# Optimization experiments

Measured on AMD Instinct MI355X. Metric: run time of the kernel, lower is better.

## Reference

```python
import jax, jax.numpy as jnp
import numpy as np

N = 100000   # num nodes
E = 1600000  # num edges
D = 128      # input_dim
K = 5        # APPNP propagation steps
EPS = 1e-8   # torch cosine_similarity eps


def setup_inputs() -> dict:
    key = jax.random.key(0)
    k1, k2, k3, k4 = jax.random.split(key, 4)
    x = jax.random.normal(k1, (N, D), jnp.float32)
    mask = jax.random.normal(k2, (N, 1), jnp.float32)
    edge_index = jax.random.randint(k3, (2, E), 0, N, dtype=jnp.int32)
    # init_t: orthogonal weight with gain sqrt(2), zero bias
    W = jax.nn.initializers.orthogonal(scale=2 ** 0.5)(k4, (D, D), jnp.float32)
    b = jnp.zeros((D,), jnp.float32)
    alpha = jnp.array(0.5, jnp.float32)
    return {"x": x, "mask": mask, "edge_index": edge_index, "W": W, "b": b, "alpha": alpha}


def reference(x, mask, edge_index, W, b, alpha):
    n = x.shape[0]
    # x_fn: Linear + Tanh
    h = jnp.tanh(x @ W.T + b)
    src, dst = edge_index[0], edge_index[1]
    hs, hd = h[src], h[dst]  # [E, D] gathers
    # torch F.cosine_similarity with eps-clamped norms
    dot = jnp.sum(hs * hd, axis=-1)
    ns = jnp.maximum(jnp.sqrt(jnp.sum(hs * hs, axis=-1)), EPS)
    nd = jnp.maximum(jnp.sqrt(jnp.sum(hd * hd, axis=-1)), EPS)
    edge_weights = jax.nn.relu(dot / (ns * nd))  # [E]

    fill = jax.nn.relu(mask)  # [N, 1]

    # PyG APPNP: gcn_norm with self loops (fill value 1.0)
    loops = jnp.arange(n, dtype=src.dtype)
    row = jnp.concatenate([src, loops])
    col = jnp.concatenate([dst, loops])
    w = jnp.concatenate([edge_weights, jnp.ones((n,), edge_weights.dtype)])
    deg = jax.ops.segment_sum(w, col, num_segments=n)
    dinv = jnp.where(deg > 0, jax.lax.rsqrt(jnp.maximum(deg, EPS)), 0.0)
    norm = dinv[row] * w * dinv[col]  # [E+N]

    # K-step APPNP: z <- (1-alpha) * A_hat z + alpha * fill
    z = fill
    for _ in range(K):
        agg = jax.ops.segment_sum(norm[:, None] * z[row], col, num_segments=n)
        z = (1.0 - alpha) * agg + alpha * fill
    return z, edge_weights
```

## Files before the change

kernel.cpp:

```cpp
#include <hip/hip_runtime.h>
#include <hip/hip_bf16.h>

typedef __attribute__((ext_vector_type(2))) float f32x2;
typedef __attribute__((ext_vector_type(4))) float f32x4;
typedef __attribute__((ext_vector_type(8))) short short8;

#define D 128
#define EPS 1e-8f
#define BSH 8
#define BSZ 256
#define SMAX 8000
#define OSH 12
#define OBK 4096

__device__ __forceinline__ unsigned int pkbf(float lo, float hi) {
    unsigned int r;
    asm("v_cvt_pk_bf16_f32 %0, %1, %2" : "=v"(r) : "v"(lo), "v"(hi));
    return r;
}

__device__ __forceinline__ float ftanh(float y) {
    float e = __builtin_amdgcn_exp2f(y * 2.885390082f);
    float r = __builtin_amdgcn_rcpf(e + 1.0f);
    return __builtin_fmaf(-2.0f, r, 1.0f);
}

__device__ __forceinline__ int dot4(unsigned int a, unsigned int b, int c) {
#if __has_builtin(__builtin_amdgcn_sdot4)
    return __builtin_amdgcn_sdot4((int)a, (int)b, c, false);
#else
    int r = c;
    r += (int)(char)(a) * (int)(char)(b);
    r += (int)(char)(a >> 8) * (int)(char)(b >> 8);
    r += (int)(char)(a >> 16) * (int)(char)(b >> 16);
    r += (int)(char)(a >> 24) * (int)(char)(b >> 24);
    return r;
#endif
}

__global__ __launch_bounds__(256) void k1_gemm_aux(const float* __restrict__ x,
                                                   const float* __restrict__ W,
                                                   const float* __restrict__ b,
                                                   signed char* __restrict__ hn8,
                                                   int N,
                                                   const float* __restrict__ mask,
                                                   float* __restrict__ fill,
                                                   const int* __restrict__ dst,
                                                   int* __restrict__ M,
                                                   int E, int nbk, int nblk, int chunk,
                                                   int gemmNB) {
    __shared__ char Wlds[D * D * 2];
    int tid = threadIdx.x;

    if (blockIdx.x >= gemmNB) {
        int baux = blockIdx.x - gemmNB;
        int* cnt = (int*)Wlds;
        for (int k = tid; k < nbk; k += 256) cnt[k] = 0;
        int fi = baux * 256 + tid;
        if (fi < N) fill[fi] = fmaxf(mask[fi], 0.0f);
        __syncthreads();
        int beg = baux * chunk, end = min(E, beg + chunk);
        for (int e = beg + tid; e < end; e += 256)
            atomicAdd(&cnt[dst[e] >> BSH], 1);
        __syncthreads();
        for (int k = tid; k < nbk; k += 256)
            M[k * nblk + baux] = cnt[k];
        return;
    }

#pragma unroll
    for (int c = 0; c < 8; ++c) {
        int i = c * 256 + tid;
        float4 lo = *(const float4*)(W + i * 8);
        float4 hi = *(const float4*)(W + i * 8 + 4);
        uint4 v;
        v.x = pkbf(lo.x, lo.y); v.y = pkbf(lo.z, lo.w);
        v.z = pkbf(hi.x, hi.y); v.w = pkbf(hi.z, hi.w);
        int byte = i << 4;
        int swz  = byte ^ (((byte >> 8) & 15) << 4);
        *(uint4*)(Wlds + swz) = v;
    }
    __syncthreads();

    int wave = tid >> 6;
    int lane = tid & 63;
    int l16  = lane & 15;
    int g    = lane >> 4;

    float bj[8];
#pragma unroll
    for (int j = 0; j < 8; ++j) bj[j] = b[j * 16 + l16];

    for (int tt = 0; tt < 2; ++tt) {
        int r0 = blockIdx.x * 128 + wave * 32 + tt * 16;
        int arow = r0 + l16;
        if (arow >= N) arow = N - 1;
        union { uint4 u; short8 s; } afr[4];
        const float* xp = x + (size_t)arow * D + g * 8;
#pragma unroll
        for (int kc = 0; kc < 4; ++kc) {
            float4 lo = *(const float4*)(xp + kc * 32);
            float4 hi = *(const float4*)(xp + kc * 32 + 4);
            afr[kc].u.x = pkbf(lo.x, lo.y);
            afr[kc].u.y = pkbf(lo.z, lo.w);
            afr[kc].u.z = pkbf(hi.x, hi.y);
            afr[kc].u.w = pkbf(hi.z, hi.w);
        }

        f32x4 acc[8];
#pragma unroll
        for (int j = 0; j < 8; ++j) acc[j] = (f32x4){0.f, 0.f, 0.f, 0.f};
#pragma unroll
        for (int j = 0; j < 8; ++j) {
#pragma unroll
            for (int kc = 0; kc < 4; ++kc) {
                int addr = (j * 16 + l16) * 256 + kc * 64 + g * 16;
                const short8* bp = (const short8*)(Wlds + (addr ^ (l16 << 4)));
                acc[j] = __builtin_amdgcn_mfma_f32_16x16x32_bf16(afr[kc].s, *bp, acc[j], 0, 0, 0);
            }
        }

        float sq[4] = {0.f, 0.f, 0.f, 0.f};
#pragma unroll
        for (int j = 0; j < 8; ++j) {
#pragma unroll
            for (int r = 0; r < 4; ++r) {
                float tv = ftanh(acc[j][r] + bj[j]);
                acc[j][r] = tv;
                sq[r] = __builtin_fmaf(tv, tv, sq[r]);
            }
        }
#pragma unroll
        for (int m = 1; m <= 8; m <<= 1) {
#pragma unroll
            for (int r = 0; r < 4; ++r) sq[r] += __shfl_xor(sq[r], m);
        }
#pragma unroll
        for (int r = 0; r < 4; ++r) {
            float inv = rsqrtf(fmaxf(sq[r], 1e-16f)) * 127.0f;
            int row = r0 + g * 4 + r;
            if (row < N) {
#pragma unroll
                for (int j = 0; j < 8; ++j) {
                    hn8[(size_t)row * D + j * 16 + l16] =
                        (signed char)__float2int_rn(acc[j][r] * inv);
                }
            }
        }
    }
}

__global__ __launch_bounds__(1024) void scan_blk(const int* __restrict__ cnt,
                                                 int* __restrict__ rp,
                                                 int* __restrict__ bsum, int nq) {
    __shared__ int wsum[16];
    __shared__ int sexcl[16];
    int tid = threadIdx.x, lane = tid & 63, wv = tid >> 6;
    int idx = blockIdx.x * 1024 + tid;
    int4 c = (idx < nq) ? ((const int4*)cnt)[idx] : make_int4(0, 0, 0, 0);
    int tsum = c.x + c.y + c.z + c.w;
    int incl = tsum;
#pragma unroll
    for (int m = 1; m < 64; m <<= 1) {
        int t = __shfl_up(incl, m);
        if (lane >= m) incl += t;
    }
    if (lane == 63) wsum[wv] = incl;
    __syncthreads();
    if (tid == 0) {
        int acc = 0;
#pragma unroll
        for (int k = 0; k < 16; ++k) { int t = wsum[k]; sexcl[k] = acc; acc += t; }
        bsum[blockIdx.x] = acc;
    }
    __syncthreads();
    int excl = sexcl[wv] + incl - tsum;
    if (idx < nq) {
        int4 r;
        r.x = excl; r.y = excl + c.x; r.z = r.y + c.y; r.w = r.z + c.z;
        ((int4*)rp)[idx] = r;
    }
}

__global__ __launch_bounds__(256) void scan_top(int* __restrict__ bsum,
                                                int* __restrict__ boff, int nbs,
                                                int* __restrict__ gcur, int nbk2) {
    for (int k = threadIdx.x; k < nbk2; k += 256) gcur[k] = k << OSH;
    if (threadIdx.x == 0) {
        int acc = 0;
        for (int k = 0; k < nbs; ++k) { int t = bsum[k]; boff[k] = acc; acc += t; }
    }
}

__global__ __launch_bounds__(256) void bscat_kernel(const int* __restrict__ src,
                                                    const int* __restrict__ dst,
                                                    const int* __restrict__ Mo,
                                                    const int* __restrict__ boff,
                                                    int2* __restrict__ ebuf,
                                                    int E, int nbk, int nblk, int chunk) {
    extern __shared__ int cur[];
    int b = blockIdx.x;
    for (int k = threadIdx.x; k < nbk; k += 256) {
        int e = k * nblk + b;
        cur[k] = Mo[e] + boff[e >> 12];
    }
    __syncthreads();
    int beg = b * chunk, end = min(E, beg + chunk);
    for (int e = beg + threadIdx.x; e < end; e += 256) {
        int d = dst[e];
        int k = d >> BSH;
        int p = atomicAdd(&cur[k], 1);
        ebuf[p] = make_int2(src[e], (e << BSH) | (d & (BSZ - 1)));
    }
}

__global__ __launch_bounds__(256) void binsort_kernel(const int* __restrict__ Mo,
                                                      const int* __restrict__ boff,
                                                      const int2* __restrict__ ebuf,
                                                      int* __restrict__ esrc,
                                                      int* __restrict__ eorig,
                                                      int* __restrict__ rp,
                                                      int E, int N, int nbk, int nblk) {
    extern __shared__ char smem[];
    int2* stage = (int2*)smem;
    int*  cnt   = (int*)(smem + SMAX * 8);
    int k = blockIdx.x;
    int eb = k * nblk;
    int base = Mo[eb] + boff[eb >> 12];
    int endb = E;
    if (k + 1 < nbk) {
        int e2 = (k + 1) * nblk;
        endb = Mo[e2] + boff[e2 >> 12];
    }
    int m = endb - base;
    if (m > SMAX) m = SMAX;

    if (threadIdx.x < BSZ) cnt[threadIdx.x] = 0;
    __syncthreads();
    for (int i = threadIdx.x; i < m; i += 256) {
        int2 v = ebuf[base + i];
        stage[i] = v;
        atomicAdd(&cnt[v.y & (BSZ - 1)], 1);
    }
    __syncthreads();
    if (threadIdx.x == 0) {
        int acc = 0;
#pragma unroll 8
        for (int t = 0; t < BSZ; ++t) { int c = cnt[t]; cnt[t] = acc; acc += c; }
    }
    __syncthreads();
    {
        int node = (k << BSH) + threadIdx.x;
        if (threadIdx.x < BSZ && node < N) rp[node] = base + cnt[threadIdx.x];
        if (k == nbk - 1 && threadIdx.x == 0) rp[N] = E;
    }
    __syncthreads();
    for (int i = threadIdx.x; i < m; i += 256) {
        int2 v = stage[i];
        int p = atomicAdd(&cnt[v.y & (BSZ - 1)], 1);
        esrc[base + p]  = v.x;
        eorig[base + p] = v.y >> BSH;
    }
}

__global__ __launch_bounds__(256) void weight_kernel(const int* __restrict__ rp,
                                                     const int* __restrict__ esrc,
                                                     const signed char* __restrict__ hn8,
                                                     float* __restrict__ warr,
                                                     float* __restrict__ dinv, int N) {
    const float SC = 1.0f / 16129.0f;
    int gid = (blockIdx.x * 256 + threadIdx.x) >> 3;
    int l   = threadIdx.x & 7;
    if (gid >= N) return;
    const uint4* hp = (const uint4*)hn8;
    uint4 dv = hp[(size_t)gid * 8 + l];
    int beg = rp[gid], end = rp[gid + 1];
    float sum = 0.f;
    int s = beg;
    for (; s + 7 < end; s += 8) {
        uint4 u[8];
        int dd[8];
#pragma unroll
        for (int q = 0; q < 8; ++q) u[q] = hp[(size_t)esrc[s + q] * 8 + l];
#pragma unroll
        for (int q = 0; q < 8; ++q) {
            int d0 = dot4(u[q].x, dv.x, 0); d0 = dot4(u[q].y, dv.y, d0);
            d0 = dot4(u[q].z, dv.z, d0);    d0 = dot4(u[q].w, dv.w, d0);
            dd[q] = d0;
        }
#pragma unroll
        for (int m = 4; m >= 1; m >>= 1) {
#pragma unroll
            for (int q = 0; q < 8; ++q) dd[q] += __shfl_xor(dd[q], m);
        }
        float wv[8];
#pragma unroll
        for (int q = 0; q < 8; ++q) {
            wv[q] = fmaxf((float)dd[q] * SC, 0.f);
            sum += wv[q];
        }
        if (l == 0) {
#pragma unroll
            for (int q = 0; q < 8; ++q) warr[s + q] = wv[q];
        }
    }
    for (; s < end; ++s) {
        uint4 u0 = hp[(size_t)esrc[s] * 8 + l];
        int d0 = dot4(u0.x, dv.x, 0); d0 = dot4(u0.y, dv.y, d0);
        d0 = dot4(u0.z, dv.z, d0);    d0 = dot4(u0.w, dv.w, d0);
#pragma unroll
        for (int m = 4; m >= 1; m >>= 1) d0 += __shfl_xor(d0, m);
        float w0 = fmaxf((float)d0 * SC, 0.f);
        if (l == 0) warr[s] = w0;
        sum += w0;
    }
    if (l == 0) dinv[gid] = rsqrtf(1.0f + sum);
}

__global__ __launch_bounds__(256) void k6_dscat_appnp1(const int* __restrict__ eorig,
                                                       const float* __restrict__ warr,
                                                       int* __restrict__ gcur,
                                                       int2* __restrict__ pbuf,
                                                       int E, int nbk2, int chunk,
                                                       int dscatNB,
                                                       const int* __restrict__ rp,
                                                       const int* __restrict__ esrc,
                                                       int2* __restrict__ pw,
                                                       const float* __restrict__ dinv,
                                                       const float* __restrict__ fill,
                                                       const float* __restrict__ alpha,
                                                       float* __restrict__ zout, int N) {
    if (blockIdx.x < dscatNB) {
        extern __shared__ char smem[];
        int2* stage = (int2*)smem;
        int*  hist  = (int*)(smem + (size_t)chunk * 8);
        int*  lcur  = hist + nbk2;
        int b = blockIdx.x;
        for (int k = threadIdx.x; k < nbk2; k += 256) hist[k] = 0;
        __syncthreads();
        int beg = b * chunk, end = min(E, beg + chunk), m = end - beg;
        for (int i = threadIdx.x; i < m; i += 256) {
            int o = eorig[beg + i];
            float w = warr[beg + i];
            stage[i] = make_int2(o, __float_as_int(w));
            atomicAdd(&hist[o >> OSH], 1);
        }
        __syncthreads();
        for (int k = threadIdx.x; k < nbk2; k += 256) {
            int c = hist[k];
            lcur[k] = c ? atomicAdd(&gcur[k], c) : 0;
        }
        __syncthreads();
        for (int i = threadIdx.x; i < m; i += 256) {
            int2 v = stage[i];
            int p = atomicAdd(&lcur[v.x >> OSH], 1);
            pbuf[p] = v;
        }
        return;
    }
    int t = (blockIdx.x - dscatNB) * 256 + threadIdx.x;
    int i = t >> 2, l = t & 3;
    if (i >= N) return;
    int beg = rp[i], end = rp[i + 1];
    float al = alpha[0];
    float oma = 1.0f - al;
    float di = dinv[i];
    float s = 0.f;
    for (int j = beg + l; j < end; j += 4) {
        int sr = esrc[j];
        float wf = oma * warr[j] * di * dinv[sr];
        pw[j] = make_int2(sr, __float_as_int(wf));
        s += wf * fill[sr];
    }
    s += __shfl_xor(s, 1);
    s += __shfl_xor(s, 2);
    if (l == 0) {
        float fi = fill[i];
        zout[i] = al * fi + oma * di * di * fi + s;
    }
}

__global__ __launch_bounds__(256) void k7_appnp2_dfin(const int* __restrict__ rp,
                                                      const int2* __restrict__ pw,
                                                      const float* __restrict__ dinv,
                                                      const float* __restrict__ fill,
                                                      const float* __restrict__ zin,
                                                      const float* __restrict__ alpha,
                                                      float* __restrict__ zout, int N,
                                                      int appnpNB,
                                                      const int2* __restrict__ pbuf,
                                                      float* __restrict__ ew, int E) {
    if (blockIdx.x >= appnpNB) {
        int bk = blockIdx.x - appnpNB;
        int base = bk << OSH;
        int m = min(OBK, E - base);
        for (int t = threadIdx.x; t < m; t += 256) {
            int2 v = pbuf[base + t];
            ew[v.x] = __int_as_float(v.y);
        }
        return;
    }
    int t = blockIdx.x * 256 + threadIdx.x;
    int i = t >> 2, l = t & 3;
    if (i >= N) return;
    int beg = rp[i], end = rp[i + 1];
    float s = 0.f;
    for (int j = beg + l; j < end; j += 4) {
        int2 p = pw[j];
        s += __int_as_float(p.y) * zin[p.x];
    }
    s += __shfl_xor(s, 1);
    s += __shfl_xor(s, 2);
    if (l == 0) {
        float al = alpha[0];
        float di = dinv[i];
        zout[i] = al * fill[i] + (1.0f - al) * di * di * zin[i] + s;
    }
}

__global__ __launch_bounds__(256) void appnp_kernel(const int* __restrict__ rp,
                                                    const int2* __restrict__ pw,
                                                    const float* __restrict__ dinv,
                                                    const float* __restrict__ fill,
                                                    const float* __restrict__ zin,
                                                    const float* __restrict__ alpha,
                                                    float* __restrict__ zout, int N) {
    int t = blockIdx.x * 256 + threadIdx.x;
    int i = t >> 2, l = t & 3;
    if (i >= N) return;
    int beg = rp[i], end = rp[i + 1];
    float s = 0.f;
    for (int j = beg + l; j < end; j += 4) {
        int2 p = pw[j];
        s += __int_as_float(p.y) * zin[p.x];
    }
    s += __shfl_xor(s, 1);
    s += __shfl_xor(s, 2);
    if (l == 0) {
        float al = alpha[0];
        float di = dinv[i];
        zout[i] = al * fill[i] + (1.0f - al) * di * di * zin[i] + s;
    }
}

extern "C" void kernel_launch(void* const* d_in, const int* in_sizes, int n_in,
                              void* d_out, int out_size, void* d_ws, size_t ws_size,
                              hipStream_t stream) {
    const float* x     = (const float*)d_in[0];
    const float* mask  = (const float*)d_in[1];
    const int*   ei    = (const int*)d_in[2];
    const float* W     = (const float*)d_in[3];
    const float* b     = (const float*)d_in[4];
    const float* alpha = (const float*)d_in[5];

    int N = in_sizes[1];
    int E = in_sizes[2] / 2;
    const int* src = ei;
    const int* dst = ei + E;

    float* out = (float*)d_out;
    float* ew  = out + N;

    int Np = (N + 15) & ~15;

    int NBK  = (N + BSZ - 1) >> BSH;
    int NBLK = 400;
    int CHUNK = (E + NBLK - 1) / NBLK;
    int L = NBK * NBLK;

    int NBK2   = (E + OBK - 1) >> OSH;
    int NBLK2  = 400;
    int CHUNK2 = (E + NBLK2 - 1) / NBLK2;

    int GEMM_NB = (N + 127) / 128;
    int nb_n4   = ((size_t)N * 4 + 255) / 256;

    char* wsb = (char*)d_ws;
    signed char* hn8 = (signed char*)wsb;
    int2* pbuf = (int2*)wsb;
    char* p = wsb + (size_t)N * D;
    float* dinv = (float*)p;           p += (size_t)Np * 4;
    float* fill = (float*)p;           p += (size_t)Np * 4;
    float* zA   = (float*)p;           p += (size_t)Np * 4;
    float* zB   = (float*)p;           p += (size_t)Np * 4;
    int*   rp   = (int*)p;             p += (size_t)(Np + 16) * 4;
    int*   M    = (int*)p;             p += (size_t)L * 4;
    int*   Mo   = (int*)p;             p += (size_t)(L + 16) * 4;
    int*   bsum = (int*)p;             p += 64 * 4;
    int*   boff = (int*)p;             p += 64 * 4;
    int*   gcur = (int*)p;             p += 512 * 4;
    int2*  ebuf = (int2*)p;            p += (size_t)E * 8;
    int*   esrc = (int*)p;             p += (size_t)E * 4;
    int*   eorig= (int*)p;             p += (size_t)E * 4;
    float* warr = (float*)p;           p += (size_t)E * 4;
    int2*  pw   = (int2*)p;

    int nq   = L / 4;
    int nbs  = (nq + 1023) / 1024;
    int ldsA = ((NBK * 4) + 15) & ~15;
    int ldsB = SMAX * 8 + BSZ * 4;
    int ldsD = CHUNK2 * 8 + 2 * NBK2 * 4;

    k1_gemm_aux<<<GEMM_NB + NBLK, 256, 0, stream>>>(x, W, b, hn8, N, mask, fill,
                                                    dst, M, E, NBK, NBLK, CHUNK, GEMM_NB);
    scan_blk<<<nbs, 1024, 0, stream>>>(M, Mo, bsum, nq);
    scan_top<<<1, 256, 0, stream>>>(bsum, boff, nbs, gcur, NBK2);
    bscat_kernel<<<NBLK, 256, ldsA, stream>>>(src, dst, Mo, boff, ebuf, E, NBK, NBLK, CHUNK);
    binsort_kernel<<<NBK, 256, ldsB, stream>>>(Mo, boff, ebuf, esrc, eorig, rp, E, N, NBK, NBLK);

    weight_kernel<<<((size_t)N * 8 + 255) / 256, 256, 0, stream>>>(rp, esrc, hn8, warr, dinv, N);

    k6_dscat_appnp1<<<NBLK2 + nb_n4, 256, ldsD, stream>>>(eorig, warr, gcur, pbuf,
                                                          E, NBK2, CHUNK2, NBLK2,
                                                          rp, esrc, pw, dinv, fill,
                                                          alpha, zA, N);
    k7_appnp2_dfin<<<nb_n4 + NBK2, 256, 0, stream>>>(rp, pw, dinv, fill,
                                                     zA, alpha, zB, N, nb_n4,
                                                     pbuf, ew, E);

    appnp_kernel<<<nb_n4, 256, 0, stream>>>(rp, pw, dinv, fill, zB, alpha, zA, N);
    appnp_kernel<<<nb_n4, 256, 0, stream>>>(rp, pw, dinv, fill, zA, alpha, zB, N);
    appnp_kernel<<<nb_n4, 256, 0, stream>>>(rp, pw, dinv, fill, zB, alpha, out, N);
}
```

Baseline: 193.9 us.

## Fuse last three APPNP steps into cooperative kernel and double GEMM rows per block

```diff
diff --git a/kernel.cpp b/kernel.cpp
--- a/kernel.cpp
+++ b/kernel.cpp
@@ -1,5 +1,8 @@
 #include <hip/hip_runtime.h>
 #include <hip/hip_bf16.h>
+#include <hip/hip_cooperative_groups.h>
+
+namespace cg = cooperative_groups;
 
 typedef __attribute__((ext_vector_type(2))) float f32x2;
 typedef __attribute__((ext_vector_type(4))) float f32x4;
@@ -12,6 +15,7 @@
 #define SMAX 8000
 #define OSH 12
 #define OBK 4096
+#define COOP_NB 1536
 
 __device__ __forceinline__ unsigned int pkbf(float lo, float hi) {
     unsigned int r;
@@ -58,6 +62,8 @@
         for (int k = tid; k < nbk; k += 256) cnt[k] = 0;
         int fi = baux * 256 + tid;
         if (fi < N) fill[fi] = fmaxf(mask[fi], 0.0f);
+        int fi2 = (nblk + baux) * 256 + tid;
+        if (fi2 < N) fill[fi2] = fmaxf(mask[fi2], 0.0f);
         __syncthreads();
         int beg = baux * chunk, end = min(E, beg + chunk);
         for (int e = beg + tid; e < end; e += 256)
@@ -91,8 +97,8 @@
 #pragma unroll
     for (int j = 0; j < 8; ++j) bj[j] = b[j * 16 + l16];
 
-    for (int tt = 0; tt < 2; ++tt) {
-        int r0 = blockIdx.x * 128 + wave * 32 + tt * 16;
+    for (int tt = 0; tt < 4; ++tt) {
+        int r0 = blockIdx.x * 256 + wave * 64 + tt * 16;
         int arow = r0 + l16;
         if (arow >= N) arow = N - 1;
         union { uint4 u; short8 s; } afr[4];
@@ -418,29 +424,47 @@
     }
 }
 
-__global__ __launch_bounds__(256) void appnp_kernel(const int* __restrict__ rp,
-                                                    const int2* __restrict__ pw,
-                                                    const float* __restrict__ dinv,
-                                                    const float* __restrict__ fill,
-                                                    const float* __restrict__ zin,
-                                                    const float* __restrict__ alpha,
-                                                    float* __restrict__ zout, int N) {
-    int t = blockIdx.x * 256 + threadIdx.x;
-    int i = t >> 2, l = t & 3;
-    if (i >= N) return;
-    int beg = rp[i], end = rp[i + 1];
-    float s = 0.f;
-    for (int j = beg + l; j < end; j += 4) {
-        int2 p = pw[j];
-        s += __int_as_float(p.y) * zin[p.x];
-    }
-    s += __shfl_xor(s, 1);
-    s += __shfl_xor(s, 2);
-    if (l == 0) {
-        float al = alpha[0];
-        float di = dinv[i];
-        zout[i] = al * fill[i] + (1.0f - al) * di * di * zin[i] + s;
-    }
+__device__ __forceinline__ void appnp_step(const int* __restrict__ rp,
+                                           const int2* __restrict__ pw,
+                                           const float* __restrict__ dinv,
+                                           const float* __restrict__ fill,
+                                           const float* __restrict__ zin,
+                                           float* __restrict__ zout,
+                                           float al, int N, int stride) {
+    for (int t = blockIdx.x * 256 + threadIdx.x; t < N * 4; t += stride) {
+        int i = t >> 2, l = t & 3;
+        int beg = rp[i], end = rp[i + 1];
+        float s = 0.f;
+        for (int j = beg + l; j < end; j += 4) {
+            int2 p = pw[j];
+            s += __int_as_float(p.y) * zin[p.x];
+        }
+        s += __shfl_xor(s, 1);
+        s += __shfl_xor(s, 2);
+        if (l == 0) {
+            float di = dinv[i];
+            zout[i] = al * fill[i] + (1.0f - al) * di * di * zin[i] + s;
+        }
+    }
+}
+
+__global__ __launch_bounds__(256, 6) void appnp_chain(const int* __restrict__ rp,
+                                                      const int2* __restrict__ pw,
+                                                      const float* __restrict__ dinv,
+                                                      const float* __restrict__ fill,
+                                                      float* __restrict__ zA,
+                                                      float* __restrict__ zB,
+                                                      float* __restrict__ out,
+                                                      const float* __restrict__ alpha,
+                                                      int N) {
+    cg::grid_group g = cg::this_grid();
+    int stride = gridDim.x * 256;
+    float al = alpha[0];
+    appnp_step(rp, pw, dinv, fill, zB, zA, al, N, stride);
+    g.sync();
+    appnp_step(rp, pw, dinv, fill, zA, zB, al, N, stride);
+    g.sync();
+    appnp_step(rp, pw, dinv, fill, zB, out, al, N, stride);
 }
 
 extern "C" void kernel_launch(void* const* d_in, const int* in_sizes, int n_in,
@@ -472,7 +496,7 @@
     int NBLK2  = 400;
     int CHUNK2 = (E + NBLK2 - 1) / NBLK2;
 
-    int GEMM_NB = (N + 127) / 128;
+    int GEMM_NB = (N + 255) / 256;
     int nb_n4   = ((size_t)N * 4 + 255) / 256;
 
     char* wsb = (char*)d_ws;
@@ -518,7 +542,10 @@
                                                      zA, alpha, zB, N, nb_n4,
                                                      pbuf, ew, E);
 
-    appnp_kernel<<<nb_n4, 256, 0, stream>>>(rp, pw, dinv, fill, zB, alpha, zA, N);
-    appnp_kernel<<<nb_n4, 256, 0, stream>>>(rp, pw, dinv, fill, zA, alpha, zB, N);
-    appnp_kernel<<<nb_n4, 256, 0, stream>>>(rp, pw, dinv, fill, zB, alpha, out, N);
-}
+    {
+        void* args[] = {(void*)&rp, (void*)&pw, (void*)&dinv, (void*)&fill,
+                        (void*)&zA, (void*)&zB, (void*)&out, (void*)&alpha, (void*)&N};
+        hipLaunchCooperativeKernel((void*)appnp_chain, dim3(COOP_NB), dim3(256),
+                                   args, 0, stream);
+    }
+}
```

New measurement: 475.8 us. 2.45x slower.
